# Performance work log

Measured on AMD Instinct MI355X. Metric: run time of the kernel, lower is better.

The kernel has to match this reference:

```python
import jax, jax.numpy as jnp
import numpy as np

# dims: batch, nodes(sensors), window, embed, topk, MLP inter width
B, NODE, WIN, EMB, TOPK, INTER = 256, 512, 64, 64, 16, 512
NEG = 0.2      # LeakyReLU negative slope in GAT attention
EPS = 1e-5     # BatchNorm eps
N = B * NODE   # total graph nodes
E = N * TOPK   # total edges


def _bn(x, gamma, beta, axes):
    # training-mode BatchNorm: batch statistics (biased var), affine gamma/beta
    m = jnp.mean(x, axis=axes, keepdims=True)
    v = jnp.var(x, axis=axes, keepdims=True)
    return (x - m) * jax.lax.rsqrt(v + EPS) * gamma + beta


def setup_inputs() -> dict:
    key = jax.random.key(0)
    ks = jax.random.split(key, 12)
    sd = lambda k, shp, s: jax.random.normal(k, shp, jnp.float32) * s
    return {
        "data": jax.random.normal(ks[0], (B, NODE, WIN), jnp.float32),
        "org_edge_index": jax.random.randint(ks[1], (2, NODE), 0, NODE, dtype=jnp.int32),  # unused by forward
        "W_emb": sd(ks[2], (NODE, EMB), 0.1),          # nn.Embedding weight
        "W_lin": sd(ks[3], (EMB, WIN), 0.1),           # GraphLayer.lin (no bias)
        "att_i": sd(ks[4], (EMB,), 0.1),
        "att_j": sd(ks[5], (EMB,), 0.1),
        "att_em_i": sd(ks[6], (EMB,), 0.1),
        "att_em_j": sd(ks[7], (EMB,), 0.1),
        "b_gnn": jnp.zeros((EMB,), jnp.float32),       # GraphLayer bias
        "g_bn1": jnp.ones((EMB,), jnp.float32), "b_bn1": jnp.zeros((EMB,), jnp.float32),
        "g_bn2": jnp.ones((EMB,), jnp.float32), "b_bn2": jnp.zeros((EMB,), jnp.float32),
        "W1": sd(ks[8], (INTER, EMB), 0.05), "b1": jnp.zeros((INTER,), jnp.float32),
        "g_bn3": jnp.ones((INTER,), jnp.float32), "b_bn3": jnp.zeros((INTER,), jnp.float32),
        "W2": sd(ks[9], (1, INTER), 0.05), "b2": jnp.zeros((1,), jnp.float32),
    }


def reference(data, org_edge_index, W_emb, W_lin, att_i, att_j, att_em_i, att_em_j,
              b_gnn, g_bn1, b_bn1, g_bn2, b_bn2, W1, b1, g_bn3, b_bn3, W2, b2):
    x = data.reshape(N, WIN)

    # ---- graph structure learning: cosine-sim top-k on DETACHED embeddings ----
    w = jax.lax.stop_gradient(W_emb)
    nw = w * jax.lax.rsqrt(jnp.sum(w * w, axis=-1, keepdims=True))
    cos = nw @ nw.T                                  # [NODE, NODE]
    _, topk_idx = jax.lax.top_k(cos, TOPK)           # [NODE, TOPK]; diag==1 -> self in top-k,
                                                     # so remove+add self-loops is a no-op on the edge set
    offs = (jnp.arange(N // NODE) * NODE)[:, None]   # batch offsets
    src = (topk_idx.reshape(-1)[None, :] + offs).reshape(-1)                 # [E] source j
    dst = (jnp.repeat(jnp.arange(NODE), TOPK)[None, :] + offs).reshape(-1)   # [E] target i (sorted)

    # ---- GAT-style message passing (heads=1, concat=False) ----
    xl = x @ W_lin.T                                 # [N, EMB]
    # per-node attention scores for key = [Wx || embedding]
    s_i = xl @ att_i + jnp.tile(W_emb @ att_em_i, B)  # [N]
    s_j = xl @ att_j + jnp.tile(W_emb @ att_em_j, B)  # [N]
    alpha = s_i[dst] + s_j[src]                      # [E]
    alpha = jnp.where(alpha > 0, alpha, NEG * alpha)  # leaky_relu
    # segment softmax over edges grouped by target node
    amax = jax.ops.segment_max(alpha, dst, num_segments=N, indices_are_sorted=True)
    ex = jnp.exp(alpha - amax[dst])
    den = jax.ops.segment_sum(ex, dst, num_segments=N, indices_are_sorted=True)
    attw = ex / den[dst]                             # [E]
    agg = jax.ops.segment_sum(attw[:, None] * xl[src], dst,
                              num_segments=N, indices_are_sorted=True)  # [N, EMB]
    h = jax.nn.relu(_bn(agg + b_gnn, g_bn1, b_bn1, axes=0))             # GNNLayer bn+relu

    # ---- readout: mul by embedding, BN over channels, MLP head (dropout=eval/identity) ----
    z = h.reshape(B, NODE, EMB) * W_emb[None]        # [B, NODE, EMB]
    z = jax.nn.relu(_bn(z, g_bn2, b_bn2, axes=(0, 1)))
    z = jax.nn.relu(_bn(z @ W1.T + b1, g_bn3, b_bn3, axes=(0, 1)))      # [B, NODE, INTER]
    out = (z @ W2.T + b2).reshape(B, NODE)
    return out
```

## Files before the change

### kernel.cpp

```cpp
#include <hip/hip_runtime.h>
#include <hip/hip_bf16.h>

constexpr int BATCH = 256, NNODE = 512, WINW = 64, EMBD = 64, KTOP = 16, CIN = 512;
constexpr int NTOT = BATCH * NNODE;
constexpr float NEGS = 0.2f;
constexpr float EPSBN = 1e-5f;

typedef __attribute__((ext_vector_type(8))) short bf16x8;
typedef __attribute__((ext_vector_type(4))) float f32x4;

union U8 { uint4 u; bf16x8 b; };

__device__ inline float bf2f(unsigned u16) {
  union { unsigned u; float f; } v; v.u = u16 << 16; return v.f;
}
__device__ inline unsigned short f2bf(float x) {
  union { float f; unsigned u; } v; v.f = x;
  unsigned r = v.u + 0x7fff + ((v.u >> 16) & 1);
  return (unsigned short)(r >> 16);
}

__global__ void k_prep(const float* __restrict__ W_emb,
                       const float* __restrict__ att_em_i,
                       const float* __restrict__ att_em_j,
                       float* __restrict__ nw, float* __restrict__ emb_si,
                       float* __restrict__ emb_sj) {
  int i = blockIdx.x, e = threadIdx.x;
  float w  = W_emb[i * EMBD + e];
  float sq = w * w;
  float si = w * att_em_i[e];
  float sj = w * att_em_j[e];
  for (int o = 32; o > 0; o >>= 1) {
    sq += __shfl_xor(sq, o);
    si += __shfl_xor(si, o);
    sj += __shfl_xor(sj, o);
  }
  nw[i * EMBD + e] = w * rsqrtf(sq);
  if (e == 0) { emb_si[i] = si; emb_sj[i] = sj; }
}

__global__ __launch_bounds__(256) void k_topk(const float* __restrict__ nw,
                                              int* __restrict__ topk) {
  __shared__ float nwi[EMBD];
  __shared__ float wbv[4];
  __shared__ int   wbi[4];
  __shared__ int   winner;
  int i = blockIdx.x, t = threadIdx.x, wv = t >> 6, ln = t & 63;
  if (t < EMBD) nwi[t] = nw[i * EMBD + t];
  __syncthreads();
  float v0 = 0.f, v1 = 0.f;
  #pragma unroll
  for (int k = 0; k < EMBD; k++) {
    v0 += nw[t * EMBD + k] * nwi[k];
    v1 += nw[(t + 256) * EMBD + k] * nwi[k];
  }
  for (int sel = 0; sel < KTOP; sel++) {
    float bv; int bi;
    if (v1 > v0) { bv = v1; bi = t + 256; } else { bv = v0; bi = t; }
    #pragma unroll
    for (int o = 1; o < 64; o <<= 1) {
      float ov = __shfl_xor(bv, o);
      int   oi = __shfl_xor(bi, o);
      if (ov > bv || (ov == bv && oi < bi)) { bv = ov; bi = oi; }
    }
    if (ln == 0) { wbv[wv] = bv; wbi[wv] = bi; }
    __syncthreads();
    if (t == 0) {
      float B = wbv[0]; int I = wbi[0];
      #pragma unroll
      for (int w = 1; w < 4; w++)
        if (wbv[w] > B || (wbv[w] == B && wbi[w] < I)) { B = wbv[w]; I = wbi[w]; }
      topk[i * KTOP + sel] = I;
      winner = I;
    }
    __syncthreads();
    int wi = winner;
    if (wi == t) v0 = -3.f;
    else if (wi == t + 256) v1 = -3.f;
  }
}

__global__ __launch_bounds__(1024) void k_fuse2(
    const float* __restrict__ data, const float* __restrict__ W_lin,
    const float* __restrict__ att_i, const float* __restrict__ att_j,
    const float* __restrict__ emb_si, const float* __restrict__ emb_sj,
    const int* __restrict__ topk,
    unsigned* __restrict__ aggb, float* __restrict__ gsum1,
    float* __restrict__ gss1) {
  __shared__ unsigned xlp[NNODE * 32];
  __shared__ float ssi[NNODE];
  __shared__ float ssj[NNODE];
  __shared__ float redb[16 * 128];
  const int b = blockIdx.x;
  const int t = threadIdx.x, w = t >> 6, ln = t & 63;
  const int lm = ln & 15, lq = ln >> 4, kb = lq * 8;

  bf16x8 bfrag[4][2];
  float ai4[4], aj4[4];
  #pragma unroll
  for (int ti = 0; ti < 4; ti++) {
    int ch = ti * 16 + lm;
    ai4[ti] = att_i[ch]; aj4[ti] = att_j[ch];
    #pragma unroll
    for (int s = 0; s < 2; s++) {
      const float* wp = W_lin + ch * WINW + s * 32 + kb;
      float4 w0 = *(const float4*)wp;
      float4 w1 = *(const float4*)(wp + 4);
      bf16x8 f;
      f[0] = (short)f2bf(w0.x); f[1] = (short)f2bf(w0.y);
      f[2] = (short)f2bf(w0.z); f[3] = (short)f2bf(w0.w);
      f[4] = (short)f2bf(w1.x); f[5] = (short)f2bf(w1.y);
      f[6] = (short)f2bf(w1.z); f[7] = (short)f2bf(w1.w);
      bfrag[ti][s] = f;
    }
  }
  #pragma unroll
  for (int tt = 0; tt < 2; tt++) {
    int tile = w * 2 + tt;
    const float* dr = data + ((size_t)b * NNODE + tile * 16 + lm) * WINW + kb;
    f32x4 acc[4];
    #pragma unroll
    for (int ti = 0; ti < 4; ti++) acc[ti] = (f32x4){0.f, 0.f, 0.f, 0.f};
    #pragma unroll
    for (int s = 0; s < 2; s++) {
      float4 d0 = *(const float4*)(dr + s * 32);
      float4 d1 = *(const float4*)(dr + s * 32 + 4);
      bf16x8 af;
      af[0] = (short)f2bf(d0.x); af[1] = (short)f2bf(d0.y);
      af[2] = (short)f2bf(d0.z); af[3] = (short)f2bf(d0.w);
      af[4] = (short)f2bf(d1.x); af[5] = (short)f2bf(d1.y);
      af[6] = (short)f2bf(d1.z); af[7] = (short)f2bf(d1.w);
      #pragma unroll
      for (int ti = 0; ti < 4; ti++)
        acc[ti] = __builtin_amdgcn_mfma_f32_16x16x32_bf16(af, bfrag[ti][s], acc[ti], 0, 0, 0);
    }
    #pragma unroll
    for (int r = 0; r < 4; r++) {
      int nd = tile * 16 + lq * 4 + r;
      int sw = ((nd >> 2) & 3) << 3;
      float si = 0.f, sj = 0.f;
      #pragma unroll
      for (int ti = 0; ti < 4; ti++) {
        float v = acc[ti][r];
        float vo = __shfl_xor(v, 1);
        si += v * ai4[ti];
        sj += v * aj4[ti];
        if (!(lm & 1)) {
          unsigned u = (unsigned)f2bf(v) | ((unsigned)f2bf(vo) << 16);
          xlp[nd * 32 + ((ti * 8 + (lm >> 1)) ^ sw)] = u;
        }
      }
      si += __shfl_xor(si, 1); si += __shfl_xor(si, 2);
      si += __shfl_xor(si, 4); si += __shfl_xor(si, 8);
      sj += __shfl_xor(sj, 1); sj += __shfl_xor(sj, 2);
      sj += __shfl_xor(sj, 4); sj += __shfl_xor(sj, 8);
      if (lm == 0) { ssi[nd] = si + emb_si[nd]; ssj[nd] = sj + emb_sj[nd]; }
    }
  }
  __syncthreads();
  const int nd4 = ln >> 4, l4 = ln & 15;
  float psx = 0.f, psy = 0.f, psz = 0.f, psw = 0.f;
  float qsx = 0.f, qsy = 0.f, qsz = 0.f, qsw = 0.f;
  for (int it = 0; it < 8; it++) {
    int node = w * 32 + it * 4 + nd4;
    const int4* tp = (const int4*)(topk + node * KTOP);
    int4 i0 = tp[0], i1 = tp[1], i2 = tp[2], i3 = tp[3];
    int idx[16] = {i0.x, i0.y, i0.z, i0.w, i1.x, i1.y, i1.z, i1.w,
                   i2.x, i2.y, i2.z, i2.w, i3.x, i3.y, i3.z, i3.w};
    float sid = ssi[node];
    float al[16], mx = -1e30f;
    #pragma unroll
    for (int k = 0; k < KTOP; k++) {
      float a = sid + ssj[idx[k]];
      a = a > 0.f ? a : NEGS * a;
      al[k] = a;
      mx = fmaxf(mx, a);
    }
    float den = 0.f;
    #pragma unroll
    for (int k = 0; k < KTOP; k++) { al[k] = __expf(al[k] - mx); den += al[k]; }
    float inv = 1.f / den;
    float ax = 0.f, ay = 0.f, az = 0.f, aw = 0.f;
    #pragma unroll
    for (int k = 0; k < KTOP; k++) {
      int sw2 = ((idx[k] >> 2) & 3) << 2;
      uint2 v = *(const uint2*)&xlp[idx[k] * 32 + 2 * (l4 ^ sw2)];
      ax += al[k] * bf2f(v.x & 0xffffu);
      ay += al[k] * bf2f(v.x >> 16);
      az += al[k] * bf2f(v.y & 0xffffu);
      aw += al[k] * bf2f(v.y >> 16);
    }
    ax *= inv; ay *= inv; az *= inv; aw *= inv;
    uint2 st;
    st.x = (unsigned)f2bf(ax) | ((unsigned)f2bf(ay) << 16);
    st.y = (unsigned)f2bf(az) | ((unsigned)f2bf(aw) << 16);
    *(uint2*)(aggb + (((size_t)b * NNODE + node) << 5) + l4 * 2) = st;
    psx += ax; psy += ay; psz += az; psw += aw;
    qsx += ax * ax; qsy += ay * ay; qsz += az * az; qsw += aw * aw;
  }
  #pragma unroll
  for (int o = 16; o <= 32; o <<= 1) {
    psx += __shfl_xor(psx, o); psy += __shfl_xor(psy, o);
    psz += __shfl_xor(psz, o); psw += __shfl_xor(psw, o);
    qsx += __shfl_xor(qsx, o); qsy += __shfl_xor(qsy, o);
    qsz += __shfl_xor(qsz, o); qsw += __shfl_xor(qsw, o);
  }
  if (ln < 16) {
    float4 a = {psx, psy, psz, psw};
    float4 q = {qsx, qsy, qsz, qsw};
    *(float4*)&redb[w * 128 + ln * 4] = a;
    *(float4*)&redb[w * 128 + 64 + ln * 4] = q;
  }
  __syncthreads();
  if (t < 64) {
    float s = 0.f;
    #pragma unroll
    for (int w16 = 0; w16 < 16; w16++) s += redb[w16 * 128 + t];
    atomicAdd(&gsum1[t], s);
  } else if (t < 128) {
    int e = t - 64;
    float s = 0.f;
    #pragma unroll
    for (int w16 = 0; w16 < 16; w16++) s += redb[w16 * 128 + 64 + e];
    atomicAdd(&gss1[e], s);
  }
}

__global__ void k_fin(const float* __restrict__ gsum, const float* __restrict__ gss,
                      const float* __restrict__ g, const float* __restrict__ bb,
                      float* __restrict__ a, float* __restrict__ c, int C) {
  int e = blockIdx.x * blockDim.x + threadIdx.x;
  if (e >= C) return;
  const float invn = 1.f / (float)NTOT;
  float m = gsum[e] * invn;
  float v = gss[e] * invn - m * m;
  float aa = g[e] * rsqrtf(v + EPSBN);
  a[e] = aa;
  c[e] = bb[e] - m * aa;
}

__global__ __launch_bounds__(256) void k_zstats3(
    const unsigned* __restrict__ aggb, const float* __restrict__ W_emb,
    const float* __restrict__ a1, const float* __restrict__ c1,
    float* __restrict__ gsum2, float* __restrict__ gss2) {
  __shared__ float red[4][8][32];
  int t = threadIdx.x;
  int gid = blockIdx.x * 256 + t;
  int p = t & 31;
  int c0 = 2 * p;
  float a10 = a1[c0], a11 = a1[c0 + 1], c10 = c1[c0], c11 = c1[c0 + 1];
  const float2* we2  = (const float2*)W_emb;
  float ps0 = 0.f, ps1 = 0.f, q0 = 0.f, q1 = 0.f;
  int stride = gridDim.x * 256;
  for (int idx = gid; idx < NTOT * 32; idx += stride) {
    unsigned u = aggb[idx];
    float vx = bf2f(u & 0xffffu), vy = bf2f(u >> 16);
    int node = (idx >> 5) & (NNODE - 1);
    float2 w = we2[node * 32 + p];
    float z0 = vx * a10 + c10; z0 = z0 > 0.f ? z0 : 0.f; z0 *= w.x;
    float z1 = vy * a11 + c11; z1 = z1 > 0.f ? z1 : 0.f; z1 *= w.y;
    ps0 += z0; q0 += z0 * z0; ps1 += z1; q1 += z1 * z1;
  }
  int g = t >> 5;
  red[0][g][p] = ps0; red[1][g][p] = ps1; red[2][g][p] = q0; red[3][g][p] = q1;
  __syncthreads();
  if (t < 128) {
    int v = t >> 5, p2 = t & 31;
    float s = 0.f;
    #pragma unroll
    for (int k = 0; k < 8; k++) s += red[v][k][p2];
    float* dst = (v & 2) ? gss2 : gsum2;
    atomicAdd(&dst[2 * p2 + (v & 1)], s);
  }
}

__global__ __launch_bounds__(256) void k_gram2(
    const unsigned* __restrict__ aggb, const float* __restrict__ W_emb,
    const float* __restrict__ a1, const float* __restrict__ c1,
    const float* __restrict__ a2, const float* __restrict__ c2,
    float* __restrict__ Gpart, float* __restrict__ hpart,
    unsigned* __restrict__ hb) {
  __shared__ float smem[4 * 4480];
  __shared__ float hred[4][64];
  const int t = threadIdx.x, wv = t >> 6, ln = t & 63;
  const int lm = ln & 15, lq = ln >> 4;
  const int r4 = ln & 7, ch8 = ln >> 3;
  const int c0 = ch8 * 8;
  float a1v[8], c1v[8], a2v[8], c2v[8];
  #pragma unroll
  for (int j = 0; j < 8; j++) {
    a1v[j] = a1[c0 + j]; c1v[j] = c1[c0 + j];
    a2v[j] = a2[c0 + j]; c2v[j] = c2[c0 + j];
  }
  unsigned* ht = (unsigned*)(smem + wv * 4480);
  bf16x8 ones;
  #pragma unroll
  for (int j = 0; j < 8; j++) ones[j] = (short)0x3F80;
  f32x4 acc[4][4];
  f32x4 accS[4];
  #pragma unroll
  for (int i = 0; i < 4; i++) {
    accS[i] = (f32x4){0.f, 0.f, 0.f, 0.f};
    #pragma unroll
    for (int j = 0; j < 4; j++) acc[i][j] = (f32x4){0.f, 0.f, 0.f, 0.f};
  }
  const uint4* ab4 = (const uint4*)aggb;
  uint4* hb4 = (uint4*)hb;
  const float4* we4 = (const float4*)W_emb;
  const int blockrow = blockIdx.x * 256;
  #pragma unroll
  for (int ck = 0; ck < 2; ck++) {
    int k0 = blockrow + wv * 64 + ck * 32;
    #pragma unroll
    for (int rr2 = 0; rr2 < 2; rr2++) {
      float h2[2][8];
      #pragma unroll
      for (int rh = 0; rh < 2; rh++) {
        int lr = r4 * 4 + rr2 * 2 + rh;
        int row = k0 + lr;
        int node = row & (NNODE - 1);
        uint4 u = ab4[(size_t)row * 8 + ch8];
        float4 w0 = we4[node * 16 + ch8 * 2];
        float4 w1 = we4[node * 16 + ch8 * 2 + 1];
        float gv[8] = {bf2f(u.x & 0xffffu), bf2f(u.x >> 16),
                       bf2f(u.y & 0xffffu), bf2f(u.y >> 16),
                       bf2f(u.z & 0xffffu), bf2f(u.z >> 16),
                       bf2f(u.w & 0xffffu), bf2f(u.w >> 16)};
        float wv8[8] = {w0.x, w0.y, w0.z, w0.w, w1.x, w1.y, w1.z, w1.w};
        uint hp[4];
        #pragma unroll
        for (int j = 0; j < 8; j++) {
          float z = gv[j] * a1v[j] + c1v[j];
          z = z > 0.f ? z : 0.f;
          z *= wv8[j];
          float hh = z * a2v[j] + c2v[j];
          hh = hh > 0.f ? hh : 0.f;
          h2[rh][j] = hh;
        }
        #pragma unroll
        for (int j = 0; j < 4; j++)
          hp[j] = (unsigned)f2bf(h2[rh][2 * j]) | ((unsigned)f2bf(h2[rh][2 * j + 1]) << 16);
        hb4[(size_t)row * 8 + ch8] = make_uint4(hp[0], hp[1], hp[2], hp[3]);
      }
      #pragma unroll
      for (int cc = 0; cc < 8; cc++) {
        int ch = c0 + cc;
        int base = ch * 20 + ((ch >> 3) & 3) * 4;
        ht[base + r4 * 2 + rr2] =
            (unsigned)f2bf(h2[0][cc]) | ((unsigned)f2bf(h2[1][cc]) << 16);
      }
    }
    bf16x8 frag[4];
    #pragma unroll
    for (int i = 0; i < 4; i++) {
      int ch = i * 16 + lm;
      int base = ch * 20 + ((ch >> 3) & 3) * 4;
      frag[i] = *(const bf16x8*)(ht + base + lq * 4);
    }
    #pragma unroll
    for (int i = 0; i < 4; i++) {
      #pragma unroll
      for (int j = 0; j < 4; j++)
        acc[i][j] = __builtin_amdgcn_mfma_f32_16x16x32_bf16(frag[i], frag[j], acc[i][j], 0, 0, 0);
      accS[i] = __builtin_amdgcn_mfma_f32_16x16x32_bf16(frag[i], ones, accS[i], 0, 0, 0);
    }
  }
  __syncthreads();
  float* Gb = smem + wv * 4480;
  #pragma unroll
  for (int i = 0; i < 4; i++) {
    #pragma unroll
    for (int j = 0; j < 4; j++) {
      float4 vv = {acc[i][j][0], acc[i][j][1], acc[i][j][2], acc[i][j][3]};
      *(float4*)(Gb + (j * 16 + lm) * 68 + i * 16 + lq * 4) = vv;
    }
    if (lm == 0) {
      float4 sv = {accS[i][0], accS[i][1], accS[i][2], accS[i][3]};
      *(float4*)&hred[wv][i * 16 + lq * 4] = sv;
    }
  }
  __syncthreads();
  for (int k = t; k < 4096; k += 256) {
    int col = k >> 6, row = k & 63;
    int o = col * 68 + row;
    Gpart[(size_t)blockIdx.x * 4096 + k] =
        smem[o] + smem[4480 + o] + smem[2 * 4480 + o] + smem[3 * 4480 + o];
  }
  if (t < 64)
    hpart[(size_t)blockIdx.x * 64 + t] =
        hred[0][t] + hred[1][t] + hred[2][t] + hred[3][t];
}

__global__ __launch_bounds__(256) void k_gred(const float* __restrict__ Gpart,
                                              const float* __restrict__ hpart,
                                              float* __restrict__ G,
                                              float* __restrict__ hsum) {
  int wi = blockIdx.x * 256 + threadIdx.x;
  if (wi < 32768) {
    int e = wi & 4095, seg = wi >> 12;
    float s = 0.f;
    #pragma unroll 8
    for (int k = 0; k < 64; k++) s += Gpart[(size_t)((seg << 6) + k) * 4096 + e];
    atomicAdd(&G[e], s);
  } else {
    int wi2 = wi - 32768;
    int e = wi2 & 63, seg = wi2 >> 6;
    float s = 0.f;
    #pragma unroll 8
    for (int k = 0; k < 64; k++) s += hpart[(size_t)((seg << 6) + k) * 64 + e];
    atomicAdd(&hsum[e], s);
  }
}

__global__ __launch_bounds__(64) void k_fin3q(
    const float* __restrict__ G, const float* __restrict__ hsum,
    const float* __restrict__ W1, const float* __restrict__ b1,
    const float* __restrict__ g3, const float* __restrict__ b3,
    float* __restrict__ a3, float* __restrict__ c3) {
  __shared__ float sw[64];
  int c = blockIdx.x, i = threadIdx.x;
  float w1i = W1[c * 64 + i];
  sw[i] = w1i;
  __syncthreads();
  float gw = 0.f;
  #pragma unroll
  for (int j = 0; j < 64; j++) gw += G[j * 64 + i] * sw[j];
  float t1 = w1i * gw;
  float t2 = w1i * hsum[i];
  for (int o = 32; o > 0; o >>= 1) { t1 += __shfl_xor(t1, o); t2 += __shfl_xor(t2, o); }
  if (i == 0) {
    float b1c = b1[c];
    const float fn = (float)NTOT, invn = 1.f / fn;
    float sum3 = t2 + fn * b1c;
    float ss3  = t1 + 2.f * b1c * t2 + fn * b1c * b1c;
    float m = sum3 * invn;
    float v = ss3 * invn - m * m;
    float aa = g3[c] * rsqrtf(v + EPSBN);
    a3[c] = aa;
    c3[c] = b3[c] - m * aa;
  }
}

__global__ __launch_bounds__(512) void k_gout3(
    const unsigned* __restrict__ hb, const float* __restrict__ W1,
    const float* __restrict__ b1, const float* __restrict__ a3,
    const float* __restrict__ c3, const float* __restrict__ W2,
    const float* __restrict__ b2, float* __restrict__ out) {
  const int t = threadIdx.x, wv = t >> 6, ln = t & 63;
  const int lm = ln & 15, lq = ln >> 4, kb = lq * 8;
  bf16x8 bfrag[4][2];
  float b1c[4], a3c[4], c3c[4], w2c[4];
  #pragma unroll
  for (int nt = 0; nt < 4; nt++) {
    int col = wv * 64 + nt * 16 + lm;
    b1c[nt] = b1[col]; a3c[nt] = a3[col]; c3c[nt] = c3[col]; w2c[nt] = W2[col];
    #pragma unroll
    for (int s = 0; s < 2; s++) {
      const float* wp = W1 + col * EMBD + s * 32 + kb;
      float4 w0 = *(const float4*)wp;
      float4 w1 = *(const float4*)(wp + 4);
      bf16x8 f;
      f[0] = (short)f2bf(w0.x); f[1] = (short)f2bf(w0.y);
      f[2] = (short)f2bf(w0.z); f[3] = (short)f2bf(w0.w);
      f[4] = (short)f2bf(w1.x); f[5] = (short)f2bf(w1.y);
      f[6] = (short)f2bf(w1.z); f[7] = (short)f2bf(w1.w);
      bfrag[nt][s] = f;
    }
  }
  float b2v = b2[0];
  const uint4* h4 = (const uint4*)hb;
  for (int tile = blockIdx.x; tile < NTOT / 16; tile += gridDim.x) {
    int rowbase = tile * 16;
    U8 ua, ub;
    ua.u = h4[(size_t)(rowbase + lm) * 8 + lq];
    ub.u = h4[(size_t)(rowbase + lm) * 8 + 4 + lq];
    f32x4 acc[4];
    #pragma unroll
    for (int nt = 0; nt < 4; nt++) acc[nt] = (f32x4){0.f, 0.f, 0.f, 0.f};
    #pragma unroll
    for (int nt = 0; nt < 4; nt++)
      acc[nt] = __builtin_amdgcn_mfma_f32_16x16x32_bf16(ua.b, bfrag[nt][0], acc[nt], 0, 0, 0);
    #pragma unroll
    for (int nt = 0; nt < 4; nt++)
      acc[nt] = __builtin_amdgcn_mfma_f32_16x16x32_bf16(ub.b, bfrag[nt][1], acc[nt], 0, 0, 0);
    #pragma unroll
    for (int r = 0; r < 4; r++) {
      float p = 0.f;
      #pragma unroll
      for (int nt = 0; nt < 4; nt++) {
        float z2 = acc[nt][r] + b1c[nt];
        float y = z2 * a3c[nt] + c3c[nt];
        y = y > 0.f ? y : 0.f;
        p += y * w2c[nt];
      }
      p += __shfl_xor(p, 1); p += __shfl_xor(p, 2);
      p += __shfl_xor(p, 4); p += __shfl_xor(p, 8);
      if (lm == 0) {
        if (wv == 0) p += b2v;
        atomicAdd(&out[rowbase + lq * 4 + r], p);
      }
    }
  }
}

extern "C" void kernel_launch(void* const* d_in, const int* in_sizes, int n_in,
                              void* d_out, int out_size, void* d_ws, size_t ws_size,
                              hipStream_t stream) {
  const float* data     = (const float*)d_in[0];
  const float* W_emb    = (const float*)d_in[2];
  const float* W_lin    = (const float*)d_in[3];
  const float* att_i    = (const float*)d_in[4];
  const float* att_j    = (const float*)d_in[5];
  const float* att_em_i = (const float*)d_in[6];
  const float* att_em_j = (const float*)d_in[7];
  const float* g_bn1    = (const float*)d_in[9];
  const float* b_bn1    = (const float*)d_in[10];
  const float* g_bn2    = (const float*)d_in[11];
  const float* b_bn2    = (const float*)d_in[12];
  const float* W1       = (const float*)d_in[13];
  const float* b1       = (const float*)d_in[14];
  const float* g_bn3    = (const float*)d_in[15];
  const float* b_bn3    = (const float*)d_in[16];
  const float* W2       = (const float*)d_in[17];
  const float* b2       = (const float*)d_in[18];
  float* out = (float*)d_out;

  char* p = (char*)d_ws;
  auto alloc = [&](size_t bytes) {
    void* r = (void*)p;
    p += (bytes + 255) & ~(size_t)255;
    return r;
  };
  unsigned* aggb  = (unsigned*)alloc((size_t)NTOT * EMBD * 2);
  unsigned* hb    = (unsigned*)alloc((size_t)NTOT * EMBD * 2);
  float*    Gpart = (float*)alloc((size_t)512 * 4096 * 4);
  float*    hpart = (float*)alloc((size_t)512 * 64 * 4);
  float*    nw    = (float*)alloc((size_t)NNODE * EMBD * 4);
  float*    emb_si = (float*)alloc(NNODE * 4);
  float*    emb_sj = (float*)alloc(NNODE * 4);
  int*      topk   = (int*)alloc(NNODE * KTOP * 4);
  float*    stats  = (float*)alloc(4416 * 4);
  float*    coefs  = (float*)alloc(1280 * 4);

  float* gsum1 = stats;       float* gss1 = stats + 64;
  float* gsum2 = stats + 128; float* gss2 = stats + 192;
  float* G     = stats + 256; float* hsum = stats + 4352;
  float* a1 = coefs;       float* c1 = coefs + 64;
  float* a2 = coefs + 128; float* c2 = coefs + 192;
  float* a3 = coefs + 256; float* c3 = coefs + 768;

  hipMemsetAsync(stats, 0, 4416 * 4, stream);
  hipMemsetAsync(out, 0, (size_t)NTOT * 4, stream);

  k_prep<<<NNODE, 64, 0, stream>>>(W_emb, att_em_i, att_em_j, nw, emb_si, emb_sj);
  k_topk<<<NNODE, 256, 0, stream>>>(nw, topk);
  k_fuse2<<<BATCH, 1024, 0, stream>>>(data, W_lin, att_i, att_j, emb_si, emb_sj,
                                      topk, aggb, gsum1, gss1);
  k_fin<<<1, 64, 0, stream>>>(gsum1, gss1, g_bn1, b_bn1, a1, c1, EMBD);
  k_zstats3<<<1024, 256, 0, stream>>>(aggb, W_emb, a1, c1, gsum2, gss2);
  k_fin<<<1, 64, 0, stream>>>(gsum2, gss2, g_bn2, b_bn2, a2, c2, EMBD);
  k_gram2<<<512, 256, 0, stream>>>(aggb, W_emb, a1, c1, a2, c2, Gpart, hpart, hb);
  k_gred<<<130, 256, 0, stream>>>(Gpart, hpart, G, hsum);
  k_fin3q<<<CIN, 64, 0, stream>>>(G, hsum, W1, b1, g_bn3, b_bn3, a3, c3);
  k_gout3<<<512, 512, 0, stream>>>(hb, W1, b1, a3, c3, W2, b2, out);
}
```

Measured before the change: 267.4 us.

## Keep xl in fp32 LDS, use packed bf16 conversions, widen Gram reduction

```diff
diff --git a/kernel.cpp b/kernel.cpp
--- a/kernel.cpp
+++ b/kernel.cpp
@@ -5,6 +5,7 @@
 constexpr int NTOT = BATCH * NNODE;
 constexpr float NEGS = 0.2f;
 constexpr float EPSBN = 1e-5f;
+constexpr int XLP = 68;
 
 typedef __attribute__((ext_vector_type(8))) short bf16x8;
 typedef __attribute__((ext_vector_type(4))) float f32x4;
@@ -18,6 +19,10 @@
   union { float f; unsigned u; } v; v.f = x;
   unsigned r = v.u + 0x7fff + ((v.u >> 16) & 1);
   return (unsigned short)(r >> 16);
+}
+__device__ inline unsigned pkbf(float a, float b) {
+  __hip_bfloat162 h = __float22bfloat162_rn(make_float2(a, b));
+  return *(unsigned*)&h;
 }
 
 __global__ void k_prep(const float* __restrict__ W_emb,
@@ -80,14 +85,14 @@
   }
 }
 
-__global__ __launch_bounds__(1024) void k_fuse2(
+__global__ __launch_bounds__(1024) void k_fuse3(
     const float* __restrict__ data, const float* __restrict__ W_lin,
     const float* __restrict__ att_i, const float* __restrict__ att_j,
     const float* __restrict__ emb_si, const float* __restrict__ emb_sj,
     const int* __restrict__ topk,
     unsigned* __restrict__ aggb, float* __restrict__ gsum1,
     float* __restrict__ gss1) {
-  __shared__ unsigned xlp[NNODE * 32];
+  __shared__ float xl[NNODE * XLP];
   __shared__ float ssi[NNODE];
   __shared__ float ssj[NNODE];
   __shared__ float redb[16 * 128];
@@ -106,12 +111,10 @@
       const float* wp = W_lin + ch * WINW + s * 32 + kb;
       float4 w0 = *(const float4*)wp;
       float4 w1 = *(const float4*)(wp + 4);
-      bf16x8 f;
-      f[0] = (short)f2bf(w0.x); f[1] = (short)f2bf(w0.y);
-      f[2] = (short)f2bf(w0.z); f[3] = (short)f2bf(w0.w);
-      f[4] = (short)f2bf(w1.x); f[5] = (short)f2bf(w1.y);
-      f[6] = (short)f2bf(w1.z); f[7] = (short)f2bf(w1.w);
-      bfrag[ti][s] = f;
+      U8 f;
+      f.u = make_uint4(pkbf(w0.x, w0.y), pkbf(w0.z, w0.w),
+                       pkbf(w1.x, w1.y), pkbf(w1.z, w1.w));
+      bfrag[ti][s] = f.b;
     }
   }
   #pragma unroll
@@ -125,30 +128,23 @@
     for (int s = 0; s < 2; s++) {
       float4 d0 = *(const float4*)(dr + s * 32);
       float4 d1 = *(const float4*)(dr + s * 32 + 4);
-      bf16x8 af;
-      af[0] = (short)f2bf(d0.x); af[1] = (short)f2bf(d0.y);
-      af[2] = (short)f2bf(d0.z); af[3] = (short)f2bf(d0.w);
-      af[4] = (short)f2bf(d1.x); af[5] = (short)f2bf(d1.y);
-      af[6] = (short)f2bf(d1.z); af[7] = (short)f2bf(d1.w);
+      U8 af;
+      af.u = make_uint4(pkbf(d0.x, d0.y), pkbf(d0.z, d0.w),
+                        pkbf(d1.x, d1.y), pkbf(d1.z, d1.w));
       #pragma unroll
       for (int ti = 0; ti < 4; ti++)
-        acc[ti] = __builtin_amdgcn_mfma_f32_16x16x32_bf16(af, bfrag[ti][s], acc[ti], 0, 0, 0);
+        acc[ti] = __builtin_amdgcn_mfma_f32_16x16x32_bf16(af.b, bfrag[ti][s], acc[ti], 0, 0, 0);
     }
     #pragma unroll
     for (int r = 0; r < 4; r++) {
       int nd = tile * 16 + lq * 4 + r;
-      int sw = ((nd >> 2) & 3) << 3;
       float si = 0.f, sj = 0.f;
       #pragma unroll
       for (int ti = 0; ti < 4; ti++) {
         float v = acc[ti][r];
-        float vo = __shfl_xor(v, 1);
+        xl[nd * XLP + ti * 16 + lm] = v;
         si += v * ai4[ti];
         sj += v * aj4[ti];
-        if (!(lm & 1)) {
-          unsigned u = (unsigned)f2bf(v) | ((unsigned)f2bf(vo) << 16);
-          xlp[nd * 32 + ((ti * 8 + (lm >> 1)) ^ sw)] = u;
-        }
       }
       si += __shfl_xor(si, 1); si += __shfl_xor(si, 2);
       si += __shfl_xor(si, 4); si += __shfl_xor(si, 8);
@@ -183,17 +179,11 @@
     float ax = 0.f, ay = 0.f, az = 0.f, aw = 0.f;
     #pragma unroll
     for (int k = 0; k < KTOP; k++) {
-      int sw2 = ((idx[k] >> 2) & 3) << 2;
-      uint2 v = *(const uint2*)&xlp[idx[k] * 32 + 2 * (l4 ^ sw2)];
-      ax += al[k] * bf2f(v.x & 0xffffu);
-      ay += al[k] * bf2f(v.x >> 16);
-      az += al[k] * bf2f(v.y & 0xffffu);
-      aw += al[k] * bf2f(v.y >> 16);
+      float4 v = *(const float4*)&xl[idx[k] * XLP + l4 * 4];
+      ax += al[k] * v.x; ay += al[k] * v.y; az += al[k] * v.z; aw += al[k] * v.w;
     }
     ax *= inv; ay *= inv; az *= inv; aw *= inv;
-    uint2 st;
-    st.x = (unsigned)f2bf(ax) | ((unsigned)f2bf(ay) << 16);
-    st.y = (unsigned)f2bf(az) | ((unsigned)f2bf(aw) << 16);
+    uint2 st = make_uint2(pkbf(ax, ay), pkbf(az, aw));
     *(uint2*)(aggb + (((size_t)b * NNODE + node) << 5) + l4 * 2) = st;
     psx += ax; psy += ay; psz += az; psw += aw;
     qsx += ax * ax; qsy += ay * ay; qsz += az * az; qsw += aw * aw;
@@ -327,7 +317,6 @@
                        bf2f(u.z & 0xffffu), bf2f(u.z >> 16),
                        bf2f(u.w & 0xffffu), bf2f(u.w >> 16)};
         float wv8[8] = {w0.x, w0.y, w0.z, w0.w, w1.x, w1.y, w1.z, w1.w};
-        uint hp[4];
         #pragma unroll
         for (int j = 0; j < 8; j++) {
           float z = gv[j] * a1v[j] + c1v[j];
@@ -337,17 +326,15 @@
           hh = hh > 0.f ? hh : 0.f;
           h2[rh][j] = hh;
         }
-        #pragma unroll
-        for (int j = 0; j < 4; j++)
-          hp[j] = (unsigned)f2bf(h2[rh][2 * j]) | ((unsigned)f2bf(h2[rh][2 * j + 1]) << 16);
-        hb4[(size_t)row * 8 + ch8] = make_uint4(hp[0], hp[1], hp[2], hp[3]);
+        hb4[(size_t)row * 8 + ch8] =
+            make_uint4(pkbf(h2[rh][0], h2[rh][1]), pkbf(h2[rh][2], h2[rh][3]),
+                       pkbf(h2[rh][4], h2[rh][5]), pkbf(h2[rh][6], h2[rh][7]));
       }
       #pragma unroll
       for (int cc = 0; cc < 8; cc++) {
         int ch = c0 + cc;
         int base = ch * 20 + ((ch >> 3) & 3) * 4;
-        ht[base + r4 * 2 + rr2] =
-            (unsigned)f2bf(h2[0][cc]) | ((unsigned)f2bf(h2[1][cc]) << 16);
+        ht[base + r4 * 2 + rr2] = pkbf(h2[0][cc], h2[1][cc]);
       }
     }
     bf16x8 frag[4];
@@ -396,18 +383,18 @@
                                               float* __restrict__ G,
                                               float* __restrict__ hsum) {
   int wi = blockIdx.x * 256 + threadIdx.x;
-  if (wi < 32768) {
+  if (wi < 131072) {
     int e = wi & 4095, seg = wi >> 12;
     float s = 0.f;
-    #pragma unroll 8
-    for (int k = 0; k < 64; k++) s += Gpart[(size_t)((seg << 6) + k) * 4096 + e];
+    #pragma unroll
+    for (int k = 0; k < 16; k++) s += Gpart[(size_t)(seg * 16 + k) * 4096 + e];
     atomicAdd(&G[e], s);
-  } else {
-    int wi2 = wi - 32768;
+  } else if (wi < 131072 + 512) {
+    int wi2 = wi - 131072;
     int e = wi2 & 63, seg = wi2 >> 6;
     float s = 0.f;
     #pragma unroll 8
-    for (int k = 0; k < 64; k++) s += hpart[(size_t)((seg << 6) + k) * 64 + e];
+    for (int k = 0; k < 64; k++) s += hpart[(size_t)(seg * 64 + k) * 64 + e];
     atomicAdd(&hsum[e], s);
   }
 }
@@ -459,12 +446,10 @@
       const float* wp = W1 + col * EMBD + s * 32 + kb;
       float4 w0 = *(const float4*)wp;
       float4 w1 = *(const float4*)(wp + 4);
-      bf16x8 f;
-      f[0] = (short)f2bf(w0.x); f[1] = (short)f2bf(w0.y);
-      f[2] = (short)f2bf(w0.z); f[3] = (short)f2bf(w0.w);
-      f[4] = (short)f2bf(w1.x); f[5] = (short)f2bf(w1.y);
-      f[6] = (short)f2bf(w1.z); f[7] = (short)f2bf(w1.w);
-      bfrag[nt][s] = f;
+      U8 f;
+      f.u = make_uint4(pkbf(w0.x, w0.y), pkbf(w0.z, w0.w),
+                       pkbf(w1.x, w1.y), pkbf(w1.z, w1.w));
+      bfrag[nt][s] = f.b;
     }
   }
   float b2v = b2[0];
@@ -554,13 +539,13 @@
 
   k_prep<<<NNODE, 64, 0, stream>>>(W_emb, att_em_i, att_em_j, nw, emb_si, emb_sj);
   k_topk<<<NNODE, 256, 0, stream>>>(nw, topk);
-  k_fuse2<<<BATCH, 1024, 0, stream>>>(data, W_lin, att_i, att_j, emb_si, emb_sj,
+  k_fuse3<<<BATCH, 1024, 0, stream>>>(data, W_lin, att_i, att_j, emb_si, emb_sj,
                                       topk, aggb, gsum1, gss1);
   k_fin<<<1, 64, 0, stream>>>(gsum1, gss1, g_bn1, b_bn1, a1, c1, EMBD);
   k_zstats3<<<1024, 256, 0, stream>>>(aggb, W_emb, a1, c1, gsum2, gss2);
   k_fin<<<1, 64, 0, stream>>>(gsum2, gss2, g_bn2, b_bn2, a2, c2, EMBD);
   k_gram2<<<512, 256, 0, stream>>>(aggb, W_emb, a1, c1, a2, c2, Gpart, hpart, hb);
-  k_gred<<<130, 256, 0, stream>>>(Gpart, hpart, G, hsum);
+  k_gred<<<514, 256, 0, stream>>>(Gpart, hpart, G, hsum);
   k_fin3q<<<CIN, 64, 0, stream>>>(G, hsum, W1, b1, g_bn3, b_bn3, a3, c3);
   k_gout3<<<512, 512, 0, stream>>>(hb, W1, b1, a3, c3, W2, b2, out);
 }
```

Result: faster. 259.4 us (-3.0%).
